# Optimization experiments

Hardware: AMD Instinct MI355X
Metric: run time of the kernel (lower is better)

The kernel has to match this reference:

```python
import jax, jax.numpy as jnp
import numpy as np

ALPHA = 0.8
B = 32768

def setup_inputs() -> dict:
    key = jax.random.key(0)
    ks = jax.random.split(key, 18)
    def w(k, shape, fan_in):
        return (jax.random.normal(k, shape, dtype=jnp.float32) / np.sqrt(fan_in)).astype(jnp.float32)
    return {
        "f1_norm": jax.random.normal(ks[0], (B, 1, 768), dtype=jnp.float32),
        "f2_norm": jax.random.normal(ks[1], (B, 1, 600), dtype=jnp.float32),
        "W_enc1": w(ks[2], (64, 768), 768), "b_enc1": jnp.zeros((64,), jnp.float32),
        "W_enc2": w(ks[3], (64, 600), 600), "b_enc2": jnp.zeros((64,), jnp.float32),
        "W_aff_a": w(ks[4], (8, 2), 2), "W_aff_v": w(ks[5], (8, 2), 2),
        "W_a": w(ks[6], (32, 64), 64), "W_v": w(ks[7], (32, 64), 64),
        "W_ca": w(ks[8], (32, 8), 8), "W_cv": w(ks[9], (32, 8), 8),
        "W_ha": w(ks[10], (8, 32), 32), "W_hv": w(ks[11], (8, 32), 32),
        "W_r1": w(ks[12], (128, 1024), 1024), "b_r1": jnp.zeros((128,), jnp.float32),
        "W_r2": w(ks[13], (32, 128), 128), "b_r2": jnp.zeros((32,), jnp.float32),
    }

def reference(f1_norm, f2_norm, W_enc1, b_enc1, W_enc2, b_enc2,
              W_aff_a, W_aff_v, W_a, W_v, W_ca, W_cv, W_ha, W_hv,
              W_r1, b_r1, W_r2, b_r2):
    # Batched version of the per-sample loop. Per-sample: imu_fts [1,64], vis_fts [1,64].
    imu = f1_norm @ W_enc1.T + b_enc1            # [B,1,64]
    vis = f2_norm @ W_enc2.T + b_enc2            # [B,1,64]
    ivT = jnp.swapaxes(jnp.concatenate([imu, vis], axis=1), 1, 2)  # [B,64,2]
    a_t = ivT @ W_aff_a.T                        # [B,64,8]
    v_t = ivT @ W_aff_v.T                        # [B,64,8]
    scale = jnp.asarray(1.0 / 8.0, dtype=imu.dtype)  # 1/sqrt(64)
    imu_att = jnp.tanh((imu @ a_t) * scale)      # [B,1,8]
    vis_att = jnp.tanh((vis @ v_t) * scale)      # [B,1,8]
    H_a = jax.nn.relu(ALPHA * (imu_att @ W_ca.T + imu @ W_a.T))          # [B,1,32]
    H_v = jax.nn.relu((1.0 - ALPHA) * (vis_att @ W_cv.T + vis @ W_v.T))  # [B,1,32]
    # [B,8,1] + [B,1,64] broadcasts to [B,8,64] (matches torch broadcast in the loop)
    att_imu = ALPHA * jnp.swapaxes(H_a @ W_ha.T, 1, 2) + imu             # [B,8,64]
    att_vis = (1.0 - ALPHA) * jnp.swapaxes(H_v @ W_hv.T, 1, 2) + vis     # [B,8,64]
    feats = jnp.concatenate([att_imu, att_vis], axis=2).reshape(f1_norm.shape[0], 1024)
    h = feats @ W_r1.T + b_r1                    # [B,128]  (dropout = identity in eval)
    return h @ W_r2.T + b_r2                     # [B,32]
```

## Files before the change

kernel.cpp:

```cpp
#include <hip/hip_runtime.h>
#include <hip/hip_bf16.h>

#define ALPHA 0.8f
#define SPB 64
#define IVW 132

typedef __attribute__((ext_vector_type(8))) short bf16x8;
typedef __attribute__((ext_vector_type(8))) unsigned short ushort8;
typedef __attribute__((ext_vector_type(4))) float f32x4;

__device__ __host__ __forceinline__ unsigned short bfu(float x) {
    __hip_bfloat16 h = __float2bfloat16(x);
    return __builtin_bit_cast(unsigned short, h);
}

__global__ void prepA(const float* __restrict__ Wr1, float* __restrict__ M) {
    int idx = blockIdx.x * 256 + threadIdx.x;
    if (idx >= 144 * 128) return;
    int x = idx >> 7;
    int r = idx & 127;
    const float* row = Wr1 + (size_t)r * 1024;
    float s = 0.f;
    if (x < 64) {
        #pragma unroll
        for (int j = 0; j < 8; ++j) s += row[j * 128 + x];
    } else if (x < 128) {
        #pragma unroll
        for (int j = 0; j < 8; ++j) s += row[j * 128 + 64 + (x - 64)];
    } else if (x < 136) {
        int j = x - 128;
        for (int k = 0; k < 64; ++k) s += row[j * 128 + k];
    } else {
        int j = x - 136;
        for (int k = 0; k < 64; ++k) s += row[j * 128 + 64 + k];
    }
    M[x * 128 + r] = s;
}

__global__ void prepB(const float* __restrict__ M, const float* __restrict__ Wr2,
                      const float* __restrict__ br1, const float* __restrict__ br2,
                      float* __restrict__ G, float* __restrict__ c) {
    int idx = blockIdx.x * 256 + threadIdx.x;
    if (idx < 144 * 32) {
        int x = idx >> 5, o = idx & 31;
        const float* m = M + x * 128;
        const float* w = Wr2 + o * 128;
        float s = 0.f;
        for (int r = 0; r < 128; ++r) s = fmaf(m[r], w[r], s);
        G[x * 32 + o] = s;
    } else if (idx < 144 * 32 + 32) {
        int o = idx - 144 * 32;
        const float* w = Wr2 + o * 128;
        float s = br2[o];
        for (int r = 0; r < 128; ++r) s = fmaf(br1[r], w[r], s);
        c[o] = s;
    }
}

__global__ void prepW(const float* __restrict__ We1, const float* __restrict__ We2,
                      unsigned short* __restrict__ Wb1, unsigned short* __restrict__ Wb2) {
    int i = blockIdx.x * 256 + threadIdx.x;
    if (i < 64 * 768) Wb1[i] = bfu(We1[i]);
    if (i < 64 * 640) {
        int r = i / 640, k = i - r * 640;
        Wb2[i] = (k < 600) ? bfu(We2[r * 600 + k]) : (unsigned short)0;
    }
}

template <int ROWLEN, int KLEN, int KPAD>
__device__ __forceinline__ void encMF(const float* __restrict__ X, const unsigned short* __restrict__ Wb,
                                      const float* __restrict__ bias,
                                      short* sA, short* sW, float* sIV,
                                      int colbase, int s0, int t) {
    const int w = t >> 6, l = t & 63;
    const int mb = 16 * (w & 3), nb = 32 * (w >> 2);
    const int r16 = l & 15, kg = l >> 4;
    const int sr = t >> 3, sc = t & 7;
    const int sphys = sc ^ (sr & 7);
    const float* xrow = X + (size_t)(s0 + sr) * ROWLEN;
    const unsigned short* wrow = Wb + sr * KPAD;

    f32x4 acc0 = {0.f, 0.f, 0.f, 0.f}, acc1 = {0.f, 0.f, 0.f, 0.f};

    const int arow = mb + r16;
    const int n0 = nb + r16, n1 = nb + 16 + r16;

    for (int kc = 0; kc < KPAD; kc += 64) {
        __syncthreads();
        const int k0 = kc + sc * 8;
        ushort8 pa;
        #pragma unroll
        for (int j = 0; j < 8; ++j) pa[j] = 0;
        if (KLEN == KPAD || k0 < KLEN) {
            const float4 u = *(const float4*)(xrow + k0);
            const float4 v = *(const float4*)(xrow + k0 + 4);
            pa[0] = bfu(u.x); pa[1] = bfu(u.y); pa[2] = bfu(u.z); pa[3] = bfu(u.w);
            pa[4] = bfu(v.x); pa[5] = bfu(v.y); pa[6] = bfu(v.z); pa[7] = bfu(v.w);
        }
        *(ushort8*)((char*)sA + sr * 128 + sphys * 16) = pa;
        *(ushort8*)((char*)sW + sr * 128 + sphys * 16) = *(const ushort8*)(wrow + k0);
        __syncthreads();
        #pragma unroll
        for (int ks = 0; ks < 2; ++ks) {
            const int ca = kg + 4 * ks;
            const bf16x8 af = *(const bf16x8*)((const char*)sA + arow * 128 + ((ca ^ (arow & 7)) * 16));
            const bf16x8 b0 = *(const bf16x8*)((const char*)sW + n0 * 128 + ((ca ^ (n0 & 7)) * 16));
            const bf16x8 b1 = *(const bf16x8*)((const char*)sW + n1 * 128 + ((ca ^ (n1 & 7)) * 16));
            acc0 = __builtin_amdgcn_mfma_f32_16x16x32_bf16(af, b0, acc0, 0, 0, 0);
            acc1 = __builtin_amdgcn_mfma_f32_16x16x32_bf16(af, b1, acc1, 0, 0, 0);
        }
    }
    const int rr = 4 * (l >> 4);
    #pragma unroll
    for (int reg = 0; reg < 4; ++reg) {
        const int row = mb + rr + reg;
        sIV[row * IVW + colbase + nb + r16]      = acc0[reg] + bias[nb + r16];
        sIV[row * IVW + colbase + nb + 16 + r16] = acc1[reg] + bias[nb + 16 + r16];
    }
}

__global__ __launch_bounds__(512, 4)
void mica_main(const float* __restrict__ f1, const float* __restrict__ f2,
               const unsigned short* __restrict__ Wb1, const unsigned short* __restrict__ Wb2,
               const float* __restrict__ be1, const float* __restrict__ be2,
               const float* __restrict__ Waffa, const float* __restrict__ Waffv,
               const float* __restrict__ Wa, const float* __restrict__ Wv,
               const float* __restrict__ Wca, const float* __restrict__ Wcv,
               const float* __restrict__ Wha, const float* __restrict__ Whv,
               const float* __restrict__ G, const float* __restrict__ cvec,
               float* __restrict__ out) {
    __shared__ float sIV[SPB * IVW];
    __shared__ float scratch[8192];
    short* sA = (short*)scratch;
    short* sW = (short*)scratch + 4096;
    const int t = threadIdx.x;
    const int s0 = blockIdx.x * SPB;

    encMF<768, 768, 768>(f1, Wb1, be1, sA, sW, sIV, 0, s0, t);
    encMF<600, 600, 640>(f2, Wb2, be2, sA, sW, sIV, 64, s0, t);
    __syncthreads();

    const int s = t & 63;
    const int q = t >> 6;
    const float* iv = sIV + s * IVW;
    float* red = scratch;

    float sii, siv, svv;
    {
        const f32x4 a0 = *(const f32x4*)(iv + q * 8);
        const f32x4 a1 = *(const f32x4*)(iv + q * 8 + 4);
        const f32x4 b0 = *(const f32x4*)(iv + 64 + q * 8);
        const f32x4 b1 = *(const f32x4*)(iv + 64 + q * 8 + 4);
        sii = a0[0]*a0[0]; siv = a0[0]*b0[0]; svv = b0[0]*b0[0];
        #pragma unroll
        for (int j = 1; j < 4; ++j) {
            sii = fmaf(a0[j], a0[j], sii); siv = fmaf(a0[j], b0[j], siv); svv = fmaf(b0[j], b0[j], svv);
        }
        #pragma unroll
        for (int j = 0; j < 4; ++j) {
            sii = fmaf(a1[j], a1[j], sii); siv = fmaf(a1[j], b1[j], siv); svv = fmaf(b1[j], b1[j], svv);
        }
    }
    red[(q * 3 + 0) * 64 + s] = sii;
    red[(q * 3 + 1) * 64 + s] = siv;
    red[(q * 3 + 2) * 64 + s] = svv;
    __syncthreads();
    sii = 0.f; siv = 0.f; svv = 0.f;
    #pragma unroll
    for (int g = 0; g < 8; ++g) {
        sii += red[(g * 3 + 0) * 64 + s];
        siv += red[(g * 3 + 1) * 64 + s];
        svv += red[(g * 3 + 2) * 64 + s];
    }

    float ia[8], va[8];
    #pragma unroll
    for (int j = 0; j < 8; ++j) {
        ia[j] = tanhf((sii * Waffa[j * 2 + 0] + siv * Waffa[j * 2 + 1]) * 0.125f);
        va[j] = tanhf((siv * Waffv[j * 2 + 0] + svv * Waffv[j * 2 + 1]) * 0.125f);
    }

    float Ha[4], Hv[4];
    #pragma unroll
    for (int mi = 0; mi < 4; ++mi) {
        const int m = q * 4 + mi;
        float sa = 0.f, sv = 0.f;
        #pragma unroll
        for (int j = 0; j < 8; ++j) {
            sa = fmaf(ia[j], Wca[m * 8 + j], sa);
            sv = fmaf(va[j], Wcv[m * 8 + j], sv);
        }
        Ha[mi] = sa; Hv[mi] = sv;
    }
    for (int k4 = 0; k4 < 64; k4 += 4) {
        const f32x4 a4 = *(const f32x4*)(iv + k4);
        const f32x4 b4 = *(const f32x4*)(iv + 64 + k4);
        #pragma unroll
        for (int mi = 0; mi < 4; ++mi) {
            const int m = q * 4 + mi;
            const f32x4 wa = *(const f32x4*)(Wa + m * 64 + k4);
            const f32x4 wv = *(const f32x4*)(Wv + m * 64 + k4);
            #pragma unroll
            for (int j = 0; j < 4; ++j) {
                Ha[mi] = fmaf(a4[j], wa[j], Ha[mi]);
                Hv[mi] = fmaf(b4[j], wv[j], Hv[mi]);
            }
        }
    }
    #pragma unroll
    for (int mi = 0; mi < 4; ++mi) {
        Ha[mi] = fmaxf(ALPHA * Ha[mi], 0.f);
        Hv[mi] = fmaxf((1.f - ALPHA) * Hv[mi], 0.f);
    }

    __syncthreads();

    #pragma unroll
    for (int j = 0; j < 8; ++j) {
        float hap = 0.f, hvp = 0.f;
        #pragma unroll
        for (int mi = 0; mi < 4; ++mi) {
            hap = fmaf(Ha[mi], Wha[j * 32 + q * 4 + mi], hap);
            hvp = fmaf(Hv[mi], Whv[j * 32 + q * 4 + mi], hvp);
        }
        red[(q * 16 + j) * 64 + s] = hap;
        red[(q * 16 + 8 + j) * 64 + s] = hvp;
    }
    __syncthreads();
    float ha[8], hv[8];
    #pragma unroll
    for (int j = 0; j < 8; ++j) {
        float sa = 0.f, sv = 0.f;
        #pragma unroll
        for (int g = 0; g < 8; ++g) {
            sa += red[(g * 16 + j) * 64 + s];
            sv += red[(g * 16 + 8 + j) * 64 + s];
        }
        ha[j] = sa; hv[j] = sv;
    }

    float o4[4];
    #pragma unroll
    for (int oi = 0; oi < 4; ++oi) o4[oi] = cvec[q * 4 + oi];
    for (int k4 = 0; k4 < 128; k4 += 4) {
        const f32x4 a4 = *(const f32x4*)(iv + k4);
        const f32x4 g0 = *(const f32x4*)(G + (k4 + 0) * 32 + q * 4);
        const f32x4 g1 = *(const f32x4*)(G + (k4 + 1) * 32 + q * 4);
        const f32x4 g2 = *(const f32x4*)(G + (k4 + 2) * 32 + q * 4);
        const f32x4 g3 = *(const f32x4*)(G + (k4 + 3) * 32 + q * 4);
        #pragma unroll
        for (int oi = 0; oi < 4; ++oi) {
            o4[oi] = fmaf(a4[0], g0[oi], o4[oi]);
            o4[oi] = fmaf(a4[1], g1[oi], o4[oi]);
            o4[oi] = fmaf(a4[2], g2[oi], o4[oi]);
            o4[oi] = fmaf(a4[3], g3[oi], o4[oi]);
        }
    }
    #pragma unroll
    for (int j = 0; j < 8; ++j) {
        const float aj = ALPHA * ha[j];
        const float vj = (1.f - ALPHA) * hv[j];
        const f32x4 gja = *(const f32x4*)(G + (128 + j) * 32 + q * 4);
        const f32x4 gjv = *(const f32x4*)(G + (136 + j) * 32 + q * 4);
        #pragma unroll
        for (int oi = 0; oi < 4; ++oi) {
            o4[oi] = fmaf(aj, gja[oi], o4[oi]);
            o4[oi] = fmaf(vj, gjv[oi], o4[oi]);
        }
    }
    f32x4 ov = {o4[0], o4[1], o4[2], o4[3]};
    *(f32x4*)(out + (size_t)(s0 + s) * 32 + q * 4) = ov;
}

extern "C" void kernel_launch(void* const* d_in, const int* in_sizes, int n_in,
                              void* d_out, int out_size, void* d_ws, size_t ws_size,
                              hipStream_t stream) {
    const float* f1    = (const float*)d_in[0];
    const float* f2    = (const float*)d_in[1];
    const float* We1   = (const float*)d_in[2];
    const float* be1   = (const float*)d_in[3];
    const float* We2   = (const float*)d_in[4];
    const float* be2   = (const float*)d_in[5];
    const float* Waffa = (const float*)d_in[6];
    const float* Waffv = (const float*)d_in[7];
    const float* Wa    = (const float*)d_in[8];
    const float* Wv    = (const float*)d_in[9];
    const float* Wca   = (const float*)d_in[10];
    const float* Wcv   = (const float*)d_in[11];
    const float* Wha   = (const float*)d_in[12];
    const float* Whv   = (const float*)d_in[13];
    const float* Wr1   = (const float*)d_in[14];
    const float* br1   = (const float*)d_in[15];
    const float* Wr2   = (const float*)d_in[16];
    const float* br2   = (const float*)d_in[17];
    float* outp = (float*)d_out;

    const int Btot = in_sizes[0] / 768;

    float* M = (float*)d_ws;
    float* G = (float*)((char*)d_ws + 73728);
    float* c = (float*)((char*)d_ws + 92160);
    unsigned short* Wb1 = (unsigned short*)((char*)d_ws + 92288);
    unsigned short* Wb2 = (unsigned short*)((char*)d_ws + 190592);

    prepA<<<(144 * 128 + 255) / 256, 256, 0, stream>>>(Wr1, M);
    prepB<<<(144 * 32 + 32 + 255) / 256, 256, 0, stream>>>(M, Wr2, br1, br2, G, c);
    prepW<<<(64 * 768 + 255) / 256, 256, 0, stream>>>(We1, We2, Wb1, Wb2);
    mica_main<<<Btot / SPB, 512, 0, stream>>>(f1, f2, Wb1, Wb2, be1, be2,
                                              Waffa, Waffv, Wa, Wv, Wca, Wcv, Wha, Whv,
                                              G, c, outp);
}
```

Before: 98.35 us.

## Load activations directly into MFMA registers, stage only weights in LDS with 256 threads

The encoder GEMM now has each wave load its 16 activation rows straight from global memory into MFMA A fragments, converting to bf16 in registers and skipping LDS staging for activations. Only the bf16 weights go through LDS, in four larger K chunks, so there are fewer barriers. The block shrinks from 512 to 256 threads, each wave computes all 64 output columns, and the tail stages are remapped to 8 outputs per thread. This is meant to cut LDS traffic and synchronisation. The cost is uncoalesced row-strided global loads and lower occupancy.

```diff
diff --git a/kernel.cpp b/kernel.cpp
--- a/kernel.cpp
+++ b/kernel.cpp
@@ -67,59 +67,90 @@
     }
 }
 
-template <int ROWLEN, int KLEN, int KPAD>
-__device__ __forceinline__ void encMF(const float* __restrict__ X, const unsigned short* __restrict__ Wb,
+template <int ROWLEN, int KPAD, int KQ, int NCH>
+__device__ __forceinline__ void encMF(const float* __restrict__ X,
+                                      const unsigned short* __restrict__ Wb,
                                       const float* __restrict__ bias,
-                                      short* sA, short* sW, float* sIV,
+                                      short* sW, float* sIV,
                                       int colbase, int s0, int t) {
     const int w = t >> 6, l = t & 63;
-    const int mb = 16 * (w & 3), nb = 32 * (w >> 2);
     const int r16 = l & 15, kg = l >> 4;
-    const int sr = t >> 3, sc = t & 7;
-    const int sphys = sc ^ (sr & 7);
-    const float* xrow = X + (size_t)(s0 + sr) * ROWLEN;
-    const unsigned short* wrow = Wb + sr * KPAD;
-
-    f32x4 acc0 = {0.f, 0.f, 0.f, 0.f}, acc1 = {0.f, 0.f, 0.f, 0.f};
-
-    const int arow = mb + r16;
-    const int n0 = nb + r16, n1 = nb + 16 + r16;
-
-    for (int kc = 0; kc < KPAD; kc += 64) {
+    const float* xrow = X + (size_t)(s0 + w * 16 + r16) * ROWLEN;
+
+    const int srow = t >> 2;
+    const int sc0 = (t & 3) * 6;
+
+    f32x4 acc0 = {0.f,0.f,0.f,0.f}, acc1 = {0.f,0.f,0.f,0.f};
+    f32x4 acc2 = {0.f,0.f,0.f,0.f}, acc3 = {0.f,0.f,0.f,0.f};
+
+    #pragma unroll
+    for (int kq = 0; kq < 4; ++kq) {
         __syncthreads();
-        const int k0 = kc + sc * 8;
-        ushort8 pa;
-        #pragma unroll
-        for (int j = 0; j < 8; ++j) pa[j] = 0;
-        if (KLEN == KPAD || k0 < KLEN) {
-            const float4 u = *(const float4*)(xrow + k0);
-            const float4 v = *(const float4*)(xrow + k0 + 4);
-            pa[0] = bfu(u.x); pa[1] = bfu(u.y); pa[2] = bfu(u.z); pa[3] = bfu(u.w);
-            pa[4] = bfu(v.x); pa[5] = bfu(v.y); pa[6] = bfu(v.z); pa[7] = bfu(v.w);
-        }
-        *(ushort8*)((char*)sA + sr * 128 + sphys * 16) = pa;
-        *(ushort8*)((char*)sW + sr * 128 + sphys * 16) = *(const ushort8*)(wrow + k0);
+        const unsigned short* wsrc = Wb + srow * KPAD + kq * KQ;
+        #pragma unroll
+        for (int j = 0; j < 6; ++j) {
+            const int c = sc0 + j;
+            const int phys = (c & 24) | ((c & 7) ^ (srow & 7));
+            ushort8 v;
+            if (KQ == 192 || c < (KQ / 8)) {
+                v = *(const ushort8*)(wsrc + c * 8);
+            } else {
+                #pragma unroll
+                for (int e = 0; e < 8; ++e) v[e] = 0;
+            }
+            *(ushort8*)((char*)sW + srow * 384 + phys * 16) = v;
+        }
         __syncthreads();
-        #pragma unroll
-        for (int ks = 0; ks < 2; ++ks) {
-            const int ca = kg + 4 * ks;
-            const bf16x8 af = *(const bf16x8*)((const char*)sA + arow * 128 + ((ca ^ (arow & 7)) * 16));
-            const bf16x8 b0 = *(const bf16x8*)((const char*)sW + n0 * 128 + ((ca ^ (n0 & 7)) * 16));
-            const bf16x8 b1 = *(const bf16x8*)((const char*)sW + n1 * 128 + ((ca ^ (n1 & 7)) * 16));
-            acc0 = __builtin_amdgcn_mfma_f32_16x16x32_bf16(af, b0, acc0, 0, 0, 0);
-            acc1 = __builtin_amdgcn_mfma_f32_16x16x32_bf16(af, b1, acc1, 0, 0, 0);
-        }
-    }
-    const int rr = 4 * (l >> 4);
+
+        #pragma unroll
+        for (int kk = 0; kk < NCH; ++kk) {
+            const int kb = kq * KQ + kk * 32 + kg * 8;
+            ushort8 pa;
+            #pragma unroll
+            for (int e = 0; e < 8; ++e) pa[e] = 0;
+            if (ROWLEN == KPAD || kb < ROWLEN) {
+                const float4 u = *(const float4*)(xrow + kb);
+                const float4 v2 = *(const float4*)(xrow + kb + 4);
+                pa[0] = bfu(u.x); pa[1] = bfu(u.y); pa[2] = bfu(u.z); pa[3] = bfu(u.w);
+                pa[4] = bfu(v2.x); pa[5] = bfu(v2.y); pa[6] = bfu(v2.z); pa[7] = bfu(v2.w);
+            }
+            const bf16x8 af = __builtin_bit_cast(bf16x8, pa);
+            const int c = kk * 4 + kg;
+            const int c24 = c & 24, c7 = c & 7;
+            {
+                const int n = r16;
+                const bf16x8 bf = *(const bf16x8*)((const char*)sW + n * 384 + (c24 | (c7 ^ (n & 7))) * 16);
+                acc0 = __builtin_amdgcn_mfma_f32_16x16x32_bf16(af, bf, acc0, 0, 0, 0);
+            }
+            {
+                const int n = 16 + r16;
+                const bf16x8 bf = *(const bf16x8*)((const char*)sW + n * 384 + (c24 | (c7 ^ (n & 7))) * 16);
+                acc1 = __builtin_amdgcn_mfma_f32_16x16x32_bf16(af, bf, acc1, 0, 0, 0);
+            }
+            {
+                const int n = 32 + r16;
+                const bf16x8 bf = *(const bf16x8*)((const char*)sW + n * 384 + (c24 | (c7 ^ (n & 7))) * 16);
+                acc2 = __builtin_amdgcn_mfma_f32_16x16x32_bf16(af, bf, acc2, 0, 0, 0);
+            }
+            {
+                const int n = 48 + r16;
+                const bf16x8 bf = *(const bf16x8*)((const char*)sW + n * 384 + (c24 | (c7 ^ (n & 7))) * 16);
+                acc3 = __builtin_amdgcn_mfma_f32_16x16x32_bf16(af, bf, acc3, 0, 0, 0);
+            }
+        }
+    }
+    const int rr = 4 * kg;
     #pragma unroll
     for (int reg = 0; reg < 4; ++reg) {
-        const int row = mb + rr + reg;
-        sIV[row * IVW + colbase + nb + r16]      = acc0[reg] + bias[nb + r16];
-        sIV[row * IVW + colbase + nb + 16 + r16] = acc1[reg] + bias[nb + 16 + r16];
-    }
-}
-
-__global__ __launch_bounds__(512, 4)
+        const int row = w * 16 + rr + reg;
+        sIV[row * IVW + colbase +  0 + r16] = acc0[reg] + bias[ 0 + r16];
+        sIV[row * IVW + colbase + 16 + r16] = acc1[reg] + bias[16 + r16];
+        sIV[row * IVW + colbase + 32 + r16] = acc2[reg] + bias[32 + r16];
+        sIV[row * IVW + colbase + 48 + r16] = acc3[reg] + bias[48 + r16];
+    }
+}
+
+__global__ __launch_bounds__(256, 2)
 void mica_main(const float* __restrict__ f1, const float* __restrict__ f2,
                const unsigned short* __restrict__ Wb1, const unsigned short* __restrict__ Wb2,
                const float* __restrict__ be1, const float* __restrict__ be2,
@@ -130,14 +161,13 @@
                const float* __restrict__ G, const float* __restrict__ cvec,
                float* __restrict__ out) {
     __shared__ float sIV[SPB * IVW];
-    __shared__ float scratch[8192];
-    short* sA = (short*)scratch;
-    short* sW = (short*)scratch + 4096;
+    __shared__ float scratch[6144];
+    short* sW = (short*)scratch;
     const int t = threadIdx.x;
     const int s0 = blockIdx.x * SPB;
 
-    encMF<768, 768, 768>(f1, Wb1, be1, sA, sW, sIV, 0, s0, t);
-    encMF<600, 600, 640>(f2, Wb2, be2, sA, sW, sIV, 64, s0, t);
+    encMF<768, 768, 192, 6>(f1, Wb1, be1, sW, sIV, 0, s0, t);
+    encMF<600, 640, 160, 5>(f2, Wb2, be2, sW, sIV, 64, s0, t);
     __syncthreads();
 
     const int s = t & 63;
@@ -145,19 +175,16 @@
     const float* iv = sIV + s * IVW;
     float* red = scratch;
 
-    float sii, siv, svv;
-    {
-        const f32x4 a0 = *(const f32x4*)(iv + q * 8);
-        const f32x4 a1 = *(const f32x4*)(iv + q * 8 + 4);
-        const f32x4 b0 = *(const f32x4*)(iv + 64 + q * 8);
-        const f32x4 b1 = *(const f32x4*)(iv + 64 + q * 8 + 4);
-        sii = a0[0]*a0[0]; siv = a0[0]*b0[0]; svv = b0[0]*b0[0];
-        #pragma unroll
-        for (int j = 1; j < 4; ++j) {
+    float sii = 0.f, siv = 0.f, svv = 0.f;
+    #pragma unroll
+    for (int h = 0; h < 2; ++h) {
+        const f32x4 a0 = *(const f32x4*)(iv + q * 16 + h * 8);
+        const f32x4 a1 = *(const f32x4*)(iv + q * 16 + h * 8 + 4);
+        const f32x4 b0 = *(const f32x4*)(iv + 64 + q * 16 + h * 8);
+        const f32x4 b1 = *(const f32x4*)(iv + 64 + q * 16 + h * 8 + 4);
+        #pragma unroll
+        for (int j = 0; j < 4; ++j) {
             sii = fmaf(a0[j], a0[j], sii); siv = fmaf(a0[j], b0[j], siv); svv = fmaf(b0[j], b0[j], svv);
-        }
-        #pragma unroll
-        for (int j = 0; j < 4; ++j) {
             sii = fmaf(a1[j], a1[j], sii); siv = fmaf(a1[j], b1[j], siv); svv = fmaf(b1[j], b1[j], svv);
         }
     }
@@ -167,7 +194,7 @@
     __syncthreads();
     sii = 0.f; siv = 0.f; svv = 0.f;
     #pragma unroll
-    for (int g = 0; g < 8; ++g) {
+    for (int g = 0; g < 4; ++g) {
         sii += red[(g * 3 + 0) * 64 + s];
         siv += red[(g * 3 + 1) * 64 + s];
         svv += red[(g * 3 + 2) * 64 + s];
@@ -180,10 +207,10 @@
         va[j] = tanhf((siv * Waffv[j * 2 + 0] + svv * Waffv[j * 2 + 1]) * 0.125f);
     }
 
-    float Ha[4], Hv[4];
-    #pragma unroll
-    for (int mi = 0; mi < 4; ++mi) {
-        const int m = q * 4 + mi;
+    float Ha[8], Hv[8];
+    #pragma unroll
+    for (int mi = 0; mi < 8; ++mi) {
+        const int m = q * 8 + mi;
         float sa = 0.f, sv = 0.f;
         #pragma unroll
         for (int j = 0; j < 8; ++j) {
@@ -196,8 +223,8 @@
         const f32x4 a4 = *(const f32x4*)(iv + k4);
         const f32x4 b4 = *(const f32x4*)(iv + 64 + k4);
         #pragma unroll
-        for (int mi = 0; mi < 4; ++mi) {
-            const int m = q * 4 + mi;
+        for (int mi = 0; mi < 8; ++mi) {
+            const int m = q * 8 + mi;
             const f32x4 wa = *(const f32x4*)(Wa + m * 64 + k4);
             const f32x4 wv = *(const f32x4*)(Wv + m * 64 + k4);
             #pragma unroll
@@ -208,7 +235,7 @@
         }
     }
     #pragma unroll
-    for (int mi = 0; mi < 4; ++mi) {
+    for (int mi = 0; mi < 8; ++mi) {
         Ha[mi] = fmaxf(ALPHA * Ha[mi], 0.f);
         Hv[mi] = fmaxf((1.f - ALPHA) * Hv[mi], 0.f);
     }
@@ -219,9 +246,9 @@
     for (int j = 0; j < 8; ++j) {
         float hap = 0.f, hvp = 0.f;
         #pragma unroll
-        for (int mi = 0; mi < 4; ++mi) {
-            hap = fmaf(Ha[mi], Wha[j * 32 + q * 4 + mi], hap);
-            hvp = fmaf(Hv[mi], Whv[j * 32 + q * 4 + mi], hvp);
+        for (int mi = 0; mi < 8; ++mi) {
+            hap = fmaf(Ha[mi], Wha[j * 32 + q * 8 + mi], hap);
+            hvp = fmaf(Hv[mi], Whv[j * 32 + q * 8 + mi], hvp);
         }
         red[(q * 16 + j) * 64 + s] = hap;
         red[(q * 16 + 8 + j) * 64 + s] = hvp;
@@ -232,44 +259,50 @@
     for (int j = 0; j < 8; ++j) {
         float sa = 0.f, sv = 0.f;
         #pragma unroll
-        for (int g = 0; g < 8; ++g) {
+        for (int g = 0; g < 4; ++g) {
             sa += red[(g * 16 + j) * 64 + s];
             sv += red[(g * 16 + 8 + j) * 64 + s];
         }
         ha[j] = sa; hv[j] = sv;
     }
 
-    float o4[4];
-    #pragma unroll
-    for (int oi = 0; oi < 4; ++oi) o4[oi] = cvec[q * 4 + oi];
+    float o8[8];
+    #pragma unroll
+    for (int oi = 0; oi < 8; ++oi) o8[oi] = cvec[q * 8 + oi];
     for (int k4 = 0; k4 < 128; k4 += 4) {
         const f32x4 a4 = *(const f32x4*)(iv + k4);
-        const f32x4 g0 = *(const f32x4*)(G + (k4 + 0) * 32 + q * 4);
-        const f32x4 g1 = *(const f32x4*)(G + (k4 + 1) * 32 + q * 4);
-        const f32x4 g2 = *(const f32x4*)(G + (k4 + 2) * 32 + q * 4);
-        const f32x4 g3 = *(const f32x4*)(G + (k4 + 3) * 32 + q * 4);
-        #pragma unroll
-        for (int oi = 0; oi < 4; ++oi) {
-            o4[oi] = fmaf(a4[0], g0[oi], o4[oi]);
-            o4[oi] = fmaf(a4[1], g1[oi], o4[oi]);
-            o4[oi] = fmaf(a4[2], g2[oi], o4[oi]);
-            o4[oi] = fmaf(a4[3], g3[oi], o4[oi]);
+        #pragma unroll
+        for (int kk = 0; kk < 4; ++kk) {
+            const f32x4 g0 = *(const f32x4*)(G + (k4 + kk) * 32 + q * 8);
+            const f32x4 g1 = *(const f32x4*)(G + (k4 + kk) * 32 + q * 8 + 4);
+            #pragma unroll
+            for (int oi = 0; oi < 4; ++oi) {
+                o8[oi]     = fmaf(a4[kk], g0[oi], o8[oi]);
+                o8[4 + oi] = fmaf(a4[kk], g1[oi], o8[4 + oi]);
+            }
         }
     }
     #pragma unroll
     for (int j = 0; j < 8; ++j) {
         const float aj = ALPHA * ha[j];
         const float vj = (1.f - ALPHA) * hv[j];
-        const f32x4 gja = *(const f32x4*)(G + (128 + j) * 32 + q * 4);
-        const f32x4 gjv = *(const f32x4*)(G + (136 + j) * 32 + q * 4);
+        const f32x4 ga0 = *(const f32x4*)(G + (128 + j) * 32 + q * 8);
+        const f32x4 ga1 = *(const f32x4*)(G + (128 + j) * 32 + q * 8 + 4);
+        const f32x4 gv0 = *(const f32x4*)(G + (136 + j) * 32 + q * 8);
+        const f32x4 gv1 = *(const f32x4*)(G + (136 + j) * 32 + q * 8 + 4);
         #pragma unroll
         for (int oi = 0; oi < 4; ++oi) {
-            o4[oi] = fmaf(aj, gja[oi], o4[oi]);
-            o4[oi] = fmaf(vj, gjv[oi], o4[oi]);
-        }
-    }
-    f32x4 ov = {o4[0], o4[1], o4[2], o4[3]};
-    *(f32x4*)(out + (size_t)(s0 + s) * 32 + q * 4) = ov;
+            o8[oi]     = fmaf(aj, ga0[oi], o8[oi]);
+            o8[4 + oi] = fmaf(aj, ga1[oi], o8[4 + oi]);
+            o8[oi]     = fmaf(vj, gv0[oi], o8[oi]);
+            o8[4 + oi] = fmaf(vj, gv1[oi], o8[4 + oi]);
+        }
+    }
+    f32x4 v0 = {o8[0], o8[1], o8[2], o8[3]};
+    f32x4 v1 = {o8[4], o8[5], o8[6], o8[7]};
+    float* op = out + (size_t)(s0 + s) * 32 + q * 8;
+    *(f32x4*)op = v0;
+    *((f32x4*)op + 1) = v1;
 }
 
 extern "C" void kernel_launch(void* const* d_in, const int* in_sizes, int n_in,
@@ -306,7 +339,7 @@
     prepA<<<(144 * 128 + 255) / 256, 256, 0, stream>>>(Wr1, M);
     prepB<<<(144 * 32 + 32 + 255) / 256, 256, 0, stream>>>(M, Wr2, br1, br2, G, c);
     prepW<<<(64 * 768 + 255) / 256, 256, 0, stream>>>(We1, We2, Wb1, Wb2);
-    mica_main<<<Btot / SPB, 512, 0, stream>>>(f1, f2, Wb1, Wb2, be1, be2,
+    mica_main<<<Btot / SPB, 256, 0, stream>>>(f1, f2, Wb1, Wb2, be1, be2,
                                               Waffa, Waffv, Wa, Wv, Wca, Wcv, Wha, Whv,
                                               G, c, outp);
 }
```

Measured after the change: 86.18 us. -12.4%, faster.
